# Optimization experiments

Hardware: AMD Instinct MI355X
Metric: run time of the kernel (lower is better)

The kernel has to match this reference:

```python
import jax, jax.numpy as jnp
import numpy as np

H = 512
N = 512
BSZ = 8
L = 4096
DIRECTION = 2  # 0=forward, 1=backward, 2=bidirectional (split N in half)


def setup_inputs() -> dict:
    key = jax.random.key(0)
    k = jax.random.split(key, 6)
    u = jax.random.normal(k[0], (BSZ, L, H), jnp.float32)
    # variable lengths in [L//2, L]
    lengths = jax.random.randint(k[1], (BSZ,), L // 2, L + 1).astype(jnp.int32)
    # LRU init: r_min=0, r_max=1, max_phase=2*pi
    u1 = jax.random.uniform(k[2], (N,), jnp.float32)
    nu_log = jnp.log(-0.5 * jnp.log(u1))
    u2 = jax.random.uniform(k[3], (N,), jnp.float32)
    theta_log = jnp.log(2.0 * np.pi * u2)
    lam = jnp.exp(-jnp.exp(nu_log) + 1j * jnp.exp(theta_log))  # (N,) complex
    gamma = jnp.sqrt(1.0 - jnp.abs(lam) ** 2)[:, None]          # (N,1)
    B = jax.random.normal(k[4], (H, N, 2), jnp.float32) / np.float32(np.sqrt(2 * H)) * gamma
    C = jax.random.normal(k[5], (2, H, N), jnp.float32) / np.float32(np.sqrt(N))
    return {"u": u, "lengths": lengths, "nu_log": nu_log, "theta_log": theta_log, "B": B, "C": C}


def _lru_scan(lam, Bu, reverse):
    """Diagonal linear recurrence x_t = lam * x_{t-1} + Bu_t along axis 2 via associative scan.
    lam: (n,) complex; Bu: (B, n, L) complex."""
    a = jnp.broadcast_to(lam[None, :, None], Bu.shape)

    def op(e1, e2):
        a1, b1 = e1
        a2, b2 = e2
        return a1 * a2, a2 * b1 + b2

    _, x = jax.lax.associative_scan(op, (a, Bu), axis=2, reverse=reverse)
    return x


def reference(u, lengths, nu_log, theta_log, B, C):
    lam = jnp.exp(-jnp.exp(nu_log) + 1j * jnp.exp(theta_log))  # (N,)
    Bc = B[..., 0] + 1j * B[..., 1]                            # (H, N) complex
    Bu = jnp.einsum('blh,hn->bnl', u, Bc)                      # (B, N, L) complex
    mask = jnp.arange(L)[None, :] < lengths[:, None]           # (B, L)
    Bu = Bu * mask[:, None, :]
    if DIRECTION == 2:
        h = N // 2
        x = jnp.concatenate([
            _lru_scan(lam[:h], Bu[:, :h], reverse=False),
            _lru_scan(lam[h:], Bu[:, h:], reverse=True),
        ], axis=1)
    elif DIRECTION == 0:
        x = _lru_scan(lam, Bu, reverse=False)
    else:
        x = _lru_scan(lam, Bu, reverse=True)
    x = x * mask[:, None, :]           # zero outputs past each sequence length
    x = jnp.swapaxes(x, 1, 2)          # (B, L, N)
    y = x.real @ C[0] - x.imag @ C[1]  # (B, L, H)  (requires H == N, as in source)
    return y
```

## Files before the change

kernel.cpp:

```cpp
#include <hip/hip_runtime.h>

#define L_SEQ   4096
#define BSZQ    8
#define ROWS    (BSZQ * L_SEQ)
#define KC1     512
#define NC1     1024
#define KC2     1024
#define NC2     512
#define CHUNK   64
#define NCHUNK  64

typedef __attribute__((ext_vector_type(8))) short bfrag;
typedef __attribute__((ext_vector_type(4))) float ffrag;

static __device__ __forceinline__ unsigned short f2bf(float f) {
    union { float f; unsigned int u; } v; v.f = f;
    unsigned int r = v.u + 0x7fffu + ((v.u >> 16) & 1u);
    return (unsigned short)(r >> 16);
}
static __device__ __forceinline__ unsigned int pk2(float a, float b) {
    return (unsigned int)f2bf(a) | ((unsigned int)f2bf(b) << 16);
}
static __device__ __forceinline__ float2 unpk2(unsigned int u) {
    union { unsigned int u; float f; } a, b;
    a.u = u << 16;
    b.u = u & 0xffff0000u;
    return make_float2(a.f, b.f);
}

static __device__ __forceinline__ void async16(const void* g, void* l) {
    __builtin_amdgcn_global_load_lds(
        (const __attribute__((address_space(1))) unsigned int*)g,
        (__attribute__((address_space(3))) unsigned int*)l,
        16, 0, 0);
}

__global__ __launch_bounds__(512) void lru_lam_kernel(
    const float* __restrict__ nu_log, const float* __restrict__ theta_log,
    float2* __restrict__ lam)
{
    int n = threadIdx.x;
    float mag = expf(-expf(nu_log[n]));
    float th  = expf(theta_log[n]);
    lam[n] = make_float2(mag * cosf(th), mag * sinf(th));
}

__global__ __launch_bounds__(256) void conv_mask_kernel(
    const float* __restrict__ u, const int* __restrict__ lengths,
    unsigned short* __restrict__ ub)
{
    int idx = blockIdx.x * 256 + threadIdx.x;
    int row = idx >> 6;
    int l = row & (L_SEQ - 1), b = row >> 12;
    bool keep = (l < lengths[b]);
    union { unsigned int s[4]; float4 f; } o;
    if (keep) {
        const float4 a = *(const float4*)(u + (size_t)idx * 8);
        const float4 c = *(const float4*)(u + (size_t)idx * 8 + 4);
        o.s[0] = pk2(a.x, a.y); o.s[1] = pk2(a.z, a.w);
        o.s[2] = pk2(c.x, c.y); o.s[3] = pk2(c.z, c.w);
    } else {
        o.s[0] = o.s[1] = o.s[2] = o.s[3] = 0u;
    }
    *(float4*)(ub + (size_t)idx * 8) = o.f;
}

__global__ __launch_bounds__(256) void prep_Bt_kernel(
    const float* __restrict__ B, unsigned short* __restrict__ Bt)
{
    int idx = blockIdx.x * 256 + threadIdx.x;
    int n2 = idx >> 9, h = idx & 511;
    Bt[idx] = f2bf(B[(size_t)h * 1024 + n2]);
}

__global__ __launch_bounds__(256) void prep_Dt_kernel(
    const float* __restrict__ C, unsigned short* __restrict__ Dt)
{
    int idx = blockIdx.x * 256 + threadIdx.x;
    int j = idx >> 10, k = idx & 1023;
    int n = k >> 1, c = k & 1;
    float v = C[((size_t)c * 512 + n) * 512 + j];
    Dt[idx] = f2bf(c ? -v : v);
}

template<int KD, int ND, bool BF16OUT>
__global__ __launch_bounds__(256) void mfma_gemm_async(
    const unsigned short* __restrict__ A,
    const unsigned short* __restrict__ Bt,
    void* __restrict__ Co)
{
    __shared__ __align__(16) char smem[32 * 132 * 4];
    uint4* As = (uint4*)smem;
    uint4* Bs = As + 512;
    float* Ts = (float*)smem;

    const int tid  = threadIdx.x;
    const int row0 = blockIdx.x * 128;
    const int col0 = blockIdx.y * 128;
    const int lane = tid & 63, w = tid >> 6;
    const int q = lane >> 4, m16 = lane & 15;
    const int wr = (w >> 1) * 64, wc = (w & 1) * 64;

    ffrag acc[4][4];
#pragma unroll
    for (int i = 0; i < 4; i++)
#pragma unroll
        for (int j = 0; j < 4; j++) acc[i][j] = (ffrag)0.f;

    for (int kt = 0; kt < KD; kt += 32) {
#pragma unroll
        for (int i = 0; i < 2; i++) {
            int t = i * 256 + w * 64 + lane;
            int r = t >> 2, kq = t & 3;
            async16(A  + (size_t)(row0 + r) * KD + kt + kq * 8, &As[i * 256 + w * 64]);
            async16(Bt + (size_t)(col0 + r) * KD + kt + kq * 8, &Bs[i * 256 + w * 64]);
        }
        __syncthreads();

        bfrag a[4], b[4];
#pragma unroll
        for (int ri = 0; ri < 4; ri++)
            a[ri] = *(bfrag*)&As[(wr + ri * 16 + m16) * 4 + q];
#pragma unroll
        for (int ci = 0; ci < 4; ci++)
            b[ci] = *(bfrag*)&Bs[(wc + ci * 16 + m16) * 4 + q];
#pragma unroll
        for (int ri = 0; ri < 4; ri++)
#pragma unroll
            for (int ci = 0; ci < 4; ci++)
                acc[ri][ci] = __builtin_amdgcn_mfma_f32_16x16x32_bf16(
                    a[ri], b[ci], acc[ri][ci], 0, 0, 0);
        __syncthreads();
    }

    if (BF16OUT) {
        unsigned int* Cb = (unsigned int*)Co;
        const int colc0 = col0 >> 1;
#pragma unroll
        for (int g = 0; g < 4; g++) {
            if (g) __syncthreads();
            if (wr == (g >> 1) * 64) {
                int gw = g & 1;
#pragma unroll
                for (int rj = 0; rj < 2; rj++) {
                    int ri = gw * 2 + rj;
#pragma unroll
                    for (int r4 = 0; r4 < 4; r4++) {
                        int rsl = rj * 16 + q * 4 + r4;
#pragma unroll
                        for (int ci = 0; ci < 4; ci++)
                            Ts[rsl * 132 + wc + ci * 16 + m16] = acc[ri][ci][r4];
                    }
                }
            }
            __syncthreads();
#pragma unroll
            for (int i = 0; i < 8; i++) {
                int flat = i * 256 + tid;
                int r = flat >> 6, cu = flat & 63;
                float2 v = *(float2*)&Ts[r * 132 + cu * 2];
                Cb[(size_t)(row0 + g * 32 + r) * (ND / 2) + colc0 + cu] =
                    pk2(v.x, v.y);
            }
        }
    } else {
        float* Cf = (float*)Co;
#pragma unroll
        for (int ri = 0; ri < 4; ri++)
#pragma unroll
            for (int r4 = 0; r4 < 4; r4++) {
                int row = row0 + wr + ri * 16 + q * 4 + r4;
#pragma unroll
                for (int ci = 0; ci < 4; ci++) {
                    int col = col0 + wc + ci * 16 + m16;
                    Cf[(size_t)row * ND + col] = acc[ri][ci][r4];
                }
            }
    }
}

__global__ __launch_bounds__(512) void scan_states_kernel(
    const unsigned int* __restrict__ bu, const float2* __restrict__ lam,
    float2* __restrict__ states)
{
    int n = threadIdx.x;
    int b = blockIdx.x >> 6;
    int c = blockIdx.x & 63;
    float2 lm = lam[n];
    float xr = 0.f, xi = 0.f;
    bool fwd = (n < 256);
    int l0 = fwd ? (c * CHUNK) : (c * CHUNK + CHUNK - 1);
    const unsigned int* p = bu + ((size_t)b * L_SEQ + l0) * 512 + n;
    ptrdiff_t step = fwd ? 512 : -512;
#pragma unroll 8
    for (int t = 0; t < CHUNK; t++) {
        float2 v = unpk2(*p);
        float nr = lm.x * xr - lm.y * xi + v.x;
        float ni = lm.x * xi + lm.y * xr + v.y;
        xr = nr; xi = ni;
        p += step;
    }
    states[((size_t)b * NCHUNK + c) * 512 + n] = make_float2(xr, xi);
}

__global__ __launch_bounds__(512) void scan_combine_kernel(
    const float2* __restrict__ states, float2* __restrict__ carries,
    const float2* __restrict__ lam)
{
    int n = threadIdx.x;
    int b = blockIdx.x;
    float2 lm = lam[n];
    float ar = lm.x, ai = lm.y;
#pragma unroll
    for (int i = 0; i < 6; i++) {
        float nr = ar * ar - ai * ai;
        ai = 2.f * ar * ai;
        ar = nr;
    }
    float cr = 0.f, ci = 0.f;
    bool fwd = (n < 256);
    if (fwd) {
        for (int c = 0; c < NCHUNK; c++) {
            size_t idx = ((size_t)b * NCHUNK + c) * 512 + n;
            carries[idx] = make_float2(cr, ci);
            float2 s = states[idx];
            float nr = ar * cr - ai * ci + s.x;
            float ni = ar * ci + ai * cr + s.y;
            cr = nr; ci = ni;
        }
    } else {
        for (int c = NCHUNK - 1; c >= 0; c--) {
            size_t idx = ((size_t)b * NCHUNK + c) * 512 + n;
            carries[idx] = make_float2(cr, ci);
            float2 s = states[idx];
            float nr = ar * cr - ai * ci + s.x;
            float ni = ar * ci + ai * cr + s.y;
            cr = nr; ci = ni;
        }
    }
}

__global__ __launch_bounds__(512) void scan_apply_kernel(
    unsigned int* __restrict__ bu, const float2* __restrict__ carries,
    const float2* __restrict__ lam, const int* __restrict__ lengths)
{
    int n = threadIdx.x;
    int b = blockIdx.x >> 6;
    int c = blockIdx.x & 63;
    int len = lengths[b];
    float2 lm = lam[n];
    float2 cy = carries[((size_t)b * NCHUNK + c) * 512 + n];
    bool fwd = (n < 256);
    int l0 = fwd ? (c * CHUNK) : (c * CHUNK + CHUNK - 1);
    int dl = fwd ? 1 : -1;
    unsigned int* p = bu + ((size_t)b * L_SEQ + l0) * 512 + n;
    ptrdiff_t step = fwd ? 512 : -512;
    float xr = cy.x, xi = cy.y;
    int l = l0;
#pragma unroll 8
    for (int t = 0; t < CHUNK; t++) {
        float2 v = unpk2(*p);
        float nr = lm.x * xr - lm.y * xi + v.x;
        float ni = lm.x * xi + lm.y * xr + v.y;
        xr = nr; xi = ni;
        *p = (l >= len) ? 0u : pk2(xr, xi);
        p += step; l += dl;
    }
}

extern "C" void kernel_launch(void* const* d_in, const int* in_sizes, int n_in,
                              void* d_out, int out_size, void* d_ws, size_t ws_size,
                              hipStream_t stream)
{
    const float* u        = (const float*)d_in[0];
    const int*   lengths  = (const int*)  d_in[1];
    const float* nu_log   = (const float*)d_in[2];
    const float* theta_log= (const float*)d_in[3];
    const float* B        = (const float*)d_in[4];
    const float* C        = (const float*)d_in[5];
    float* y = (float*)d_out;

    char* wp = (char*)d_ws;
    float2* lam     = (float2*)wp;  wp += 4096;
    float2* states  = (float2*)wp;  wp += (size_t)BSZQ * NCHUNK * 512 * 8;
    float2* carries = (float2*)wp;  wp += (size_t)BSZQ * NCHUNK * 512 * 8;
    unsigned int* bu = (unsigned int*)wp; wp += (size_t)ROWS * 512 * 4;
    unsigned short* ub = (unsigned short*)wp; wp += (size_t)ROWS * 512 * 2;
    unsigned short* Bt = (unsigned short*)wp; wp += (size_t)NC1 * KC1 * 2;
    unsigned short* Dt = (unsigned short*)wp; wp += (size_t)NC2 * KC2 * 2;

    lru_lam_kernel<<<1, 512, 0, stream>>>(nu_log, theta_log, lam);
    conv_mask_kernel<<<8192, 256, 0, stream>>>(u, lengths, ub);
    prep_Bt_kernel<<<2048, 256, 0, stream>>>(B, Bt);
    prep_Dt_kernel<<<2048, 256, 0, stream>>>(C, Dt);

    {
        dim3 grid(ROWS / 128, NC1 / 128);
        mfma_gemm_async<KC1, NC1, true><<<grid, 256, 0, stream>>>(ub, Bt, bu);
    }

    scan_states_kernel<<<BSZQ * NCHUNK, 512, 0, stream>>>(bu, lam, states);
    scan_combine_kernel<<<BSZQ, 512, 0, stream>>>(states, carries, lam);
    scan_apply_kernel<<<BSZQ * NCHUNK, 512, 0, stream>>>(bu, carries, lam, lengths);

    {
        dim3 grid(ROWS / 128, NC2 / 128);
        mfma_gemm_async<KC2, NC2, false><<<grid, 256, 0, stream>>>(
            (const unsigned short*)bu, Dt, y);
    }
}
```

Baseline: 298.4 us.

## Rewrite GEMMs as 256x256 eight-wave double-buffered pipelined MFMA kernel

```diff
diff --git a/kernel.cpp b/kernel.cpp
--- a/kernel.cpp
+++ b/kernel.cpp
@@ -83,97 +83,147 @@
     Dt[idx] = f2bf(c ? -v : v);
 }
 
+#define STAGE_HALF(GP, TB, HH, KT, GR0) do {                                   \
+    _Pragma("unroll")                                                          \
+    for (int j_ = 0; j_ < 2; j_++) {                                           \
+        int c_ = j_ * 512 + tid;                                               \
+        int r_ = (HH) * 128 + (c_ >> 3);                                       \
+        int sw_ = (c_ & 7) ^ (r_ & 7);                                         \
+        async16(GP + (size_t)((GR0) + r_) * KD + (KT) + sw_ * 8,               \
+                &TB[(size_t)((HH) * 1024 + j_ * 512 + w * 64) * 8]);           \
+    }                                                                          \
+} while (0)
+
+#define RD_A(H, MH, KK) do {                                                   \
+    _Pragma("unroll")                                                          \
+    for (int ri_ = 0; ri_ < 4; ri_++) {                                        \
+        int r_ = wm * 128 + (MH) * 64 + ri_ * 16 + m16;                        \
+        int cc_ = (KK) * 4 + q;                                                \
+        af[ri_] = *(const bfrag*)&As[H][(size_t)(r_ * 8 + (cc_ ^ (r_ & 7))) * 8]; \
+    }                                                                          \
+} while (0)
+
+#define RD_B(H, KK, DST) do {                                                  \
+    _Pragma("unroll")                                                          \
+    for (int ci_ = 0; ci_ < 4; ci_++) {                                        \
+        int r_ = wn * 64 + ci_ * 16 + m16;                                     \
+        int cc_ = (KK) * 4 + q;                                                \
+        DST[ci_] = *(const bfrag*)&Bs[H][(size_t)(r_ * 8 + (cc_ ^ (r_ & 7))) * 8]; \
+    }                                                                          \
+} while (0)
+
+#define MMQ(MH, BKR) do {                                                      \
+    __builtin_amdgcn_s_setprio(1);                                             \
+    _Pragma("unroll")                                                          \
+    for (int ri_ = 0; ri_ < 4; ri_++)                                          \
+    _Pragma("unroll")                                                          \
+    for (int ci_ = 0; ci_ < 4; ci_++)                                          \
+        acc[(MH) * 4 + ri_][ci_] = __builtin_amdgcn_mfma_f32_16x16x32_bf16(    \
+            af[ri_], BKR[ci_], acc[(MH) * 4 + ri_][ci_], 0, 0, 0);             \
+    __builtin_amdgcn_s_setprio(0);                                             \
+} while (0)
+
+#define BAR()   __builtin_amdgcn_s_barrier()
+#define LGKM0() do { asm volatile("s_waitcnt lgkmcnt(0)" ::: "memory");        \
+                     __builtin_amdgcn_sched_barrier(0); } while (0)
+
 template<int KD, int ND, bool BF16OUT>
-__global__ __launch_bounds__(256) void mfma_gemm_async(
+__global__ __launch_bounds__(512, 2) void mfma_gemm_8p(
     const unsigned short* __restrict__ A,
     const unsigned short* __restrict__ Bt,
     void* __restrict__ Co)
 {
-    __shared__ __align__(16) char smem[32 * 132 * 4];
-    uint4* As = (uint4*)smem;
-    uint4* Bs = As + 512;
-    float* Ts = (float*)smem;
-
-    const int tid  = threadIdx.x;
-    const int row0 = blockIdx.x * 128;
-    const int col0 = blockIdx.y * 128;
-    const int lane = tid & 63, w = tid >> 6;
+    __shared__ __align__(16) unsigned short As[2][256 * 64];
+    __shared__ __align__(16) unsigned short Bs[2][256 * 64];
+
+    const int tid = threadIdx.x;
+    const int w = tid >> 6, lane = tid & 63;
     const int q = lane >> 4, m16 = lane & 15;
-    const int wr = (w >> 1) * 64, wc = (w & 1) * 64;
-
-    ffrag acc[4][4];
-#pragma unroll
-    for (int i = 0; i < 4; i++)
+    const int wm = w >> 2, wn = w & 3;
+    const int row0 = blockIdx.x * 256;
+    const int col0 = blockIdx.y * 256;
+
+    ffrag acc[8][4];
+#pragma unroll
+    for (int i = 0; i < 8; i++)
 #pragma unroll
         for (int j = 0; j < 4; j++) acc[i][j] = (ffrag)0.f;
 
-    for (int kt = 0; kt < KD; kt += 32) {
-#pragma unroll
-        for (int i = 0; i < 2; i++) {
-            int t = i * 256 + w * 64 + lane;
-            int r = t >> 2, kq = t & 3;
-            async16(A  + (size_t)(row0 + r) * KD + kt + kq * 8, &As[i * 256 + w * 64]);
-            async16(Bt + (size_t)(col0 + r) * KD + kt + kq * 8, &Bs[i * 256 + w * 64]);
-        }
-        __syncthreads();
-
-        bfrag a[4], b[4];
-#pragma unroll
-        for (int ri = 0; ri < 4; ri++)
-            a[ri] = *(bfrag*)&As[(wr + ri * 16 + m16) * 4 + q];
-#pragma unroll
-        for (int ci = 0; ci < 4; ci++)
-            b[ci] = *(bfrag*)&Bs[(wc + ci * 16 + m16) * 4 + q];
-#pragma unroll
-        for (int ri = 0; ri < 4; ri++)
-#pragma unroll
-            for (int ci = 0; ci < 4; ci++)
-                acc[ri][ci] = __builtin_amdgcn_mfma_f32_16x16x32_bf16(
-                    a[ri], b[ci], acc[ri][ci], 0, 0, 0);
-        __syncthreads();
+    bfrag af[4], b0f[4], b1f[4];
+
+    STAGE_HALF(A,  As[0], 0, 0,  row0);
+    STAGE_HALF(A,  As[0], 1, 0,  row0);
+    STAGE_HALF(Bt, Bs[0], 0, 0,  col0);
+    STAGE_HALF(Bt, Bs[0], 1, 0,  col0);
+    STAGE_HALF(Bt, Bs[1], 0, 64, col0);
+    STAGE_HALF(Bt, Bs[1], 1, 64, col0);
+    asm volatile("s_waitcnt vmcnt(4)" ::: "memory");
+    BAR();
+
+    constexpr int NT = KD / 128;
+    for (int i = 0; i < NT; i++) {
+        const int kt = i * 128;
+        const bool nl = (i + 1 < NT);
+        RD_A(0, 0, 0); RD_B(0, 0, b0f);
+        STAGE_HALF(A, As[1], 0, kt + 64, row0);
+        BAR(); LGKM0(); MMQ(0, b0f); BAR();
+        RD_A(0, 0, 1); RD_B(0, 1, b1f);
+        STAGE_HALF(A, As[1], 1, kt + 64, row0);
+        BAR(); LGKM0(); MMQ(0, b1f); BAR();
+        RD_A(0, 1, 0);
+        if (nl) STAGE_HALF(Bt, Bs[0], 0, kt + 128, col0);
+        BAR(); LGKM0(); MMQ(1, b0f); BAR();
+        RD_A(0, 1, 1);
+        if (nl) STAGE_HALF(Bt, Bs[0], 1, kt + 128, col0);
+        BAR(); LGKM0(); MMQ(1, b1f);
+        if (nl) asm volatile("s_waitcnt vmcnt(4)" ::: "memory");
+        else    asm volatile("s_waitcnt vmcnt(0)" ::: "memory");
+        BAR();
+        RD_A(1, 0, 0); RD_B(1, 0, b0f);
+        if (nl) STAGE_HALF(A, As[0], 0, kt + 128, row0);
+        BAR(); LGKM0(); MMQ(0, b0f); BAR();
+        RD_A(1, 0, 1); RD_B(1, 1, b1f);
+        if (nl) STAGE_HALF(A, As[0], 1, kt + 128, row0);
+        BAR(); LGKM0(); MMQ(0, b1f); BAR();
+        RD_A(1, 1, 0);
+        if (nl) STAGE_HALF(Bt, Bs[1], 0, kt + 192, col0);
+        BAR(); LGKM0(); MMQ(1, b0f); BAR();
+        RD_A(1, 1, 1);
+        if (nl) STAGE_HALF(Bt, Bs[1], 1, kt + 192, col0);
+        BAR(); LGKM0(); MMQ(1, b1f);
+        if (nl) asm volatile("s_waitcnt vmcnt(4)" ::: "memory");
+        BAR();
     }
 
     if (BF16OUT) {
         unsigned int* Cb = (unsigned int*)Co;
-        const int colc0 = col0 >> 1;
-#pragma unroll
-        for (int g = 0; g < 4; g++) {
-            if (g) __syncthreads();
-            if (wr == (g >> 1) * 64) {
-                int gw = g & 1;
-#pragma unroll
-                for (int rj = 0; rj < 2; rj++) {
-                    int ri = gw * 2 + rj;
-#pragma unroll
-                    for (int r4 = 0; r4 < 4; r4++) {
-                        int rsl = rj * 16 + q * 4 + r4;
-#pragma unroll
-                        for (int ci = 0; ci < 4; ci++)
-                            Ts[rsl * 132 + wc + ci * 16 + m16] = acc[ri][ci][r4];
-                    }
+        const int colc0 = (col0 >> 1) + wn * 32;
+#pragma unroll
+        for (int ri8 = 0; ri8 < 8; ri8++)
+#pragma unroll
+            for (int cp = 0; cp < 2; cp++)
+#pragma unroll
+                for (int r4 = 0; r4 < 4; r4++) {
+                    float a0 = acc[ri8][cp * 2][r4];
+                    float a1 = acc[ri8][cp * 2 + 1][r4];
+                    float b0 = __shfl_xor(a0, 1);
+                    float b1 = __shfl_xor(a1, 1);
+                    unsigned int uo = (m16 & 1) ? pk2(b1, a1) : pk2(a0, b0);
+                    int row = row0 + wm * 128 + ri8 * 16 + q * 4 + r4;
+                    int ccol = (cp * 2 + (m16 & 1)) * 8 + (m16 >> 1);
+                    Cb[(size_t)row * (ND / 2) + colc0 + ccol] = uo;
                 }
-            }
-            __syncthreads();
-#pragma unroll
-            for (int i = 0; i < 8; i++) {
-                int flat = i * 256 + tid;
-                int r = flat >> 6, cu = flat & 63;
-                float2 v = *(float2*)&Ts[r * 132 + cu * 2];
-                Cb[(size_t)(row0 + g * 32 + r) * (ND / 2) + colc0 + cu] =
-                    pk2(v.x, v.y);
-            }
-        }
     } else {
         float* Cf = (float*)Co;
 #pragma unroll
-        for (int ri = 0; ri < 4; ri++)
+        for (int ri8 = 0; ri8 < 8; ri8++)
 #pragma unroll
             for (int r4 = 0; r4 < 4; r4++) {
-                int row = row0 + wr + ri * 16 + q * 4 + r4;
+                int row = row0 + wm * 128 + ri8 * 16 + q * 4 + r4;
 #pragma unroll
                 for (int ci = 0; ci < 4; ci++) {
-                    int col = col0 + wc + ci * 16 + m16;
-                    Cf[(size_t)row * ND + col] = acc[ri][ci][r4];
+                    int col = col0 + wn * 64 + ci * 16 + m16;
+                    Cf[(size_t)row * ND + col] = acc[ri8][ci][r4];
                 }
             }
     }
@@ -219,22 +269,19 @@
     }
     float cr = 0.f, ci = 0.f;
     bool fwd = (n < 256);
-    if (fwd) {
-        for (int c = 0; c < NCHUNK; c++) {
-            size_t idx = ((size_t)b * NCHUNK + c) * 512 + n;
-            carries[idx] = make_float2(cr, ci);
-            float2 s = states[idx];
-            float nr = ar * cr - ai * ci + s.x;
-            float ni = ar * ci + ai * cr + s.y;
-            cr = nr; ci = ni;
+    for (int g = 0; g < 8; g++) {
+        float2 s[8];
+#pragma unroll
+        for (int k = 0; k < 8; k++) {
+            int c = fwd ? (g * 8 + k) : (63 - (g * 8 + k));
+            s[k] = states[((size_t)b * NCHUNK + c) * 512 + n];
         }
-    } else {
-        for (int c = NCHUNK - 1; c >= 0; c--) {
-            size_t idx = ((size_t)b * NCHUNK + c) * 512 + n;
-            carries[idx] = make_float2(cr, ci);
-            float2 s = states[idx];
-            float nr = ar * cr - ai * ci + s.x;
-            float ni = ar * ci + ai * cr + s.y;
+#pragma unroll
+        for (int k = 0; k < 8; k++) {
+            int c = fwd ? (g * 8 + k) : (63 - (g * 8 + k));
+            carries[((size_t)b * NCHUNK + c) * 512 + n] = make_float2(cr, ci);
+            float nr = ar * cr - ai * ci + s[k].x;
+            float ni = ar * ci + ai * cr + s[k].y;
             cr = nr; ci = ni;
         }
     }
@@ -295,8 +342,8 @@
     prep_Dt_kernel<<<2048, 256, 0, stream>>>(C, Dt);
 
     {
-        dim3 grid(ROWS / 128, NC1 / 128);
-        mfma_gemm_async<KC1, NC1, true><<<grid, 256, 0, stream>>>(ub, Bt, bu);
+        dim3 grid(ROWS / 256, NC1 / 256);
+        mfma_gemm_8p<KC1, NC1, true><<<grid, 512, 0, stream>>>(ub, Bt, bu);
     }
 
     scan_states_kernel<<<BSZQ * NCHUNK, 512, 0, stream>>>(bu, lam, states);
@@ -304,8 +351,8 @@
     scan_apply_kernel<<<BSZQ * NCHUNK, 512, 0, stream>>>(bu, carries, lam, lengths);
 
     {
-        dim3 grid(ROWS / 128, NC2 / 128);
-        mfma_gemm_async<KC2, NC2, false><<<grid, 256, 0, stream>>>(
+        dim3 grid(ROWS / 256, NC2 / 256);
+        mfma_gemm_8p<KC2, NC2, false><<<grid, 512, 0, stream>>>(
             (const unsigned short*)bu, Dt, y);
     }
 }
```

After: 270.8 us. 1.1x faster.
